# Kernel tuning notes

Measured on AMD Instinct MI355X. Metric: run time of the kernel, lower is better.

The kernel has to match this reference:

```python
import jax, jax.numpy as jnp
import numpy as np

LOG2 = float(np.log(2.0))
INV_SQRT3 = float(1.0 / np.sqrt(3.0))

def ssp(x):
    # ShiftedSoftPlus: softplus(x) - log(2)
    return jax.nn.softplus(x) - LOG2

def setup_inputs() -> dict:
    key = jax.random.key(0)
    ks = jax.random.split(key, 13)
    N, E, M, A, R, H = 50000, 800000, 32, 16, 8, 64
    return {
        "node_feats": jax.random.normal(ks[0], (N, 4 * M), dtype=jnp.float32),  # 32x0e + 32x1o flat
        "node_attrs": jax.random.normal(ks[1], (N, A), dtype=jnp.float32),
        "edge_embedding": jax.random.uniform(ks[2], (E, R), dtype=jnp.float32),  # radial basis, 0e
        "edge_attrs": jax.random.normal(ks[3], (E, 4), dtype=jnp.float32),  # SH: 1x0e + 1x1o
        "edge_index": jax.random.randint(ks[4], (2, E), 0, N),
        "W1s": jax.random.normal(ks[5], (M, M), dtype=jnp.float32),
        "W1v": jax.random.normal(ks[6], (M, M), dtype=jnp.float32),
        "Wr0": jax.random.normal(ks[7], (R, H), dtype=jnp.float32),
        "Wr1": jax.random.normal(ks[8], (H, 4 * M), dtype=jnp.float32),  # tp.weight_numel = 4 paths * 32 mul
        "W2s": jax.random.normal(ks[9], (2 * M, M), dtype=jnp.float32),
        "W2v": jax.random.normal(ks[10], (2 * M, M), dtype=jnp.float32),
        "Wsc_s": jax.random.normal(ks[11], (M, A, M), dtype=jnp.float32),
        "Wsc_v": jax.random.normal(ks[12], (M, A, M), dtype=jnp.float32),
    }

def reference(node_feats, node_attrs, edge_embedding, edge_attrs, edge_index,
              W1s, W1v, Wr0, Wr1, W2s, W2v, Wsc_s, Wsc_v):
    N = node_feats.shape[0]
    M = 32           # multiplicity of each irrep
    A = node_attrs.shape[1]
    AVG_NEIGH = 16.0
    # split flat irreps features: [N,32] scalars (0e), [N,32,3] vectors (1o)
    s_in = node_feats[:, :M]
    v_in = node_feats[:, M:].reshape(N, M, 3)

    # linear_1: per-irrep channel mixing, e3nn 1/sqrt(fan_in) normalization
    inv_m = 1.0 / float(np.sqrt(M))
    s = (s_in @ W1s) * inv_m                                  # [N,32]
    v = jnp.einsum('nmc,mk->nkc', v_in, W1v) * inv_m          # [N,32,3]

    # radial MLP on edge scalars -> per-edge tensor-product path weights [E,4,32]
    h = ssp((edge_embedding @ Wr0) * (1.0 / float(np.sqrt(edge_embedding.shape[1]))))
    w = (h @ Wr1) * (1.0 / float(np.sqrt(h.shape[1])))
    w = w.reshape(-1, 4, M)
    w0, w1, w2, w3 = w[:, 0], w[:, 1], w[:, 2], w[:, 3]

    src, dst = edge_index[0], edge_index[1]
    ss = s[src]                                               # [E,32]
    vv = v[src]                                               # [E,32,3]
    e0 = edge_attrs[:, :1]                                    # [E,1]  Y_0
    e1 = edge_attrs[:, 1:4]                                   # [E,3]  Y_1

    # weighted CG tensor product, 'uvu' paths (component normalization)
    m0 = w0 * ss * e0                                                   # 0e x 0e -> 0e
    m3 = w3 * jnp.einsum('emc,ec->em', vv, e1) * INV_SQRT3              # 1o x 1o -> 0e
    m1 = w1[:, :, None] * ss[:, :, None] * e1[:, None, :]               # 0e x 1o -> 1o
    m2 = w2[:, :, None] * vv * e0[:, :, None]                           # 1o x 0e -> 1o
    mid_s = jnp.concatenate([m0, m3], axis=1)                           # [E,64]
    mid_v = jnp.concatenate([m1, m2], axis=1)                           # [E,64,3]

    # scatter-sum to destination nodes
    ns = jax.ops.segment_sum(mid_s, dst, num_segments=N)
    nv = jax.ops.segment_sum(mid_v, dst, num_segments=N)
    neigh = 1.0 / float(np.sqrt(AVG_NEIGH))

    # linear_2 on simplified mid irreps 64x0e + 64x1o
    inv2 = 1.0 / float(np.sqrt(2 * M))
    out_s = (ns @ W2s) * (inv2 * neigh)
    out_v = jnp.einsum('nmc,mk->nkc', nv, W2v) * (inv2 * neigh)

    # self connection: FullyConnectedTensorProduct(node_feats_in, node_attrs)
    fc = 1.0 / float(np.sqrt(M * A))
    out_s = out_s + jnp.einsum('nu,na,uaw->nw', s_in, node_attrs, Wsc_s) * fc
    out_v = out_v + jnp.einsum('nuc,na,uaw->nwc', v_in, node_attrs, Wsc_v) * fc

    return jnp.concatenate([out_s, out_v.reshape(N, 3 * M)], axis=1)
```

## Files before the change

### kernel.cpp

```cpp
#include <hip/hip_runtime.h>
#include <stdint.h>
#include <math.h>

typedef __attribute__((ext_vector_type(8))) short bf16x8;
typedef __attribute__((ext_vector_type(4))) short s16x4;
typedef __attribute__((ext_vector_type(4))) float f32x4;

__device__ __forceinline__ unsigned short f2bf(float f){
  unsigned int u = __float_as_uint(f);
  u += 0x7fffu + ((u >> 16) & 1u);
  return (unsigned short)(u >> 16);
}

__device__ __forceinline__ float bf2f(short s){
  return __uint_as_float(((unsigned int)(unsigned short)s) << 16);
}

__device__ __forceinline__ float ssp_f(float x){
  float u = exp2f(-fabsf(x)*1.4426950408889634f);
  return fmaxf(x, 0.f) + 0.6931471805599453f*(__log2f(1.0f + u) - 1.0f);
}

__global__ void k_count_prep(const int* __restrict__ eidx, int E, int* __restrict__ cnt,
                             const float* __restrict__ Wr0, const float* __restrict__ Wr1,
                             const float* __restrict__ Wsc_s, const float* __restrict__ Wsc_v,
                             const float* __restrict__ W1s, const float* __restrict__ W1v,
                             const float* __restrict__ W2s, const float* __restrict__ W2v,
                             unsigned short* __restrict__ wr1frag, float* __restrict__ wr0p,
                             unsigned short* __restrict__ wscfrag, unsigned short* __restrict__ w1frag,
                             unsigned short* __restrict__ w2frag){
  int id = blockIdx.x*256 + threadIdx.x;
  if(id < 512) wr0p[id] = Wr0[(id & 7)*64 + (id >> 3)];
  if(id < 1024){
    int fi = id >> 6, lane = id & 63;
    int c0 = lane & 15, g = lane >> 4;
    int kt = fi >> 3, ct = fi & 7;
    unsigned short tmp[8];
    #pragma unroll
    for(int i = 0; i < 8; i++){
      int k = kt*32 + g*8 + i;
      tmp[i] = f2bf(Wr1[k*128 + ct*16 + c0]);
    }
    #pragma unroll
    for(int i = 0; i < 8; i++) wr1frag[id*8 + i] = tmp[i];
  }
  if(id < 4096){
    int sel  = id >> 11;
    int fi   = (id >> 6) & 31;
    int lane = id & 63;
    int c0 = lane & 15, g = lane >> 4;
    int ks = fi >> 1, ct = fi & 1;
    const float* W = sel ? Wsc_v : Wsc_s;
    bf16x8 tmp;
    #pragma unroll
    for(int i = 0; i < 8; i++){
      int k = ks*32 + g*8 + i;
      tmp[i] = (short)f2bf(W[k*32 + ct*16 + c0]);
    }
    *(bf16x8*)&wscfrag[(size_t)id*8] = tmp;
  }
  if(id < 256){
    int sel = id >> 7, ct = (id >> 6) & 1, lane = id & 63;
    int c0 = lane & 15, g = lane >> 4;
    const float* W = sel ? W1v : W1s;
    bf16x8 tmp;
    #pragma unroll
    for(int i = 0; i < 8; i++){
      int m = g*8 + i;
      tmp[i] = (short)f2bf(W[m*32 + ct*16 + c0]);
    }
    *(bf16x8*)&w1frag[(size_t)id*8] = tmp;
  }
  if(id < 512){
    int fi = id >> 6, lane = id & 63;
    int c0 = lane & 15, g = lane >> 4;
    int sel = fi >> 2, kt = (fi >> 1) & 1, ct = fi & 1;
    const float* W = sel ? W2v : W2s;
    bf16x8 tmp;
    #pragma unroll
    for(int i = 0; i < 8; i++){
      int k = kt*32 + g*8 + i;
      tmp[i] = (short)f2bf(W[k*32 + ct*16 + c0]);
    }
    *(bf16x8*)&w2frag[(size_t)id*8] = tmp;
  }
  if(id < E) atomicAdd(&cnt[eidx[E + id]], 1);
}

__global__ void k_scan_a(const int* __restrict__ cnt, int N, int* __restrict__ offs, int* __restrict__ bsum){
  __shared__ int arr[1024];
  int t = threadIdx.x, i = blockIdx.x*1024 + t;
  int v = (i < N) ? cnt[i] : 0;
  int own = v;
  arr[t] = v;
  for(int off = 1; off < 1024; off <<= 1){
    __syncthreads();
    int u = (t >= off) ? arr[t - off] : 0;
    __syncthreads();
    arr[t] += u;
  }
  if(i < N) offs[i] = arr[t] - own;
  if(t == 1023) bsum[blockIdx.x] = arr[1023];
}

__global__ void k_scan_b(int* __restrict__ bsum, int NB, int* __restrict__ offs, int N){
  if(threadIdx.x == 0 && blockIdx.x == 0){
    int run = 0;
    for(int b = 0; b < NB; b++){ int t = bsum[b]; bsum[b] = run; run += t; }
    offs[N] = run;
  }
}

__global__ void k_scan_c(int* __restrict__ offs, const int* __restrict__ bsum, int* __restrict__ cursor, int N){
  int i = blockIdx.x*1024 + threadIdx.x;
  if(i < N){
    int v = offs[i] + bsum[blockIdx.x];
    offs[i] = v;
    cursor[i] = v;
  }
}

__global__ void k_perm(const float* __restrict__ eemb, const float* __restrict__ eattr,
                       const int* __restrict__ eidx, int E, int* __restrict__ cursor,
                       int* __restrict__ src_perm, float* __restrict__ eattr_perm,
                       float* __restrict__ eemb_perm){
  int e = blockIdx.x*256 + threadIdx.x;
  if(e < E){
    int d = eidx[E + e];
    int dp = atomicAdd(&cursor[d], 1);
    src_perm[dp] = eidx[e];
    *(f32x4*)(eattr_perm + (size_t)dp*4) = *(const f32x4*)(eattr + (size_t)e*4);
    *(f32x4*)(eemb_perm + (size_t)dp*8)     = *(const f32x4*)(eemb + (size_t)e*8);
    *(f32x4*)(eemb_perm + (size_t)dp*8 + 4) = *(const f32x4*)(eemb + (size_t)e*8 + 4);
  }
}

__global__ __launch_bounds__(256) void k_node(
    const float* __restrict__ nf, const float* __restrict__ na,
    const unsigned short* __restrict__ w1frag,
    const unsigned short* __restrict__ wscfrag,
    unsigned short* __restrict__ sv, float* __restrict__ out, int N)
{
  __shared__ float xl[64*133];
  __shared__ __align__(16) float al[64*20];
  const int t = threadIdx.x;
  const int n0 = blockIdx.x*64;

  for(int idx = t; idx < 64*128; idx += 256){
    int r = idx >> 7, c = idx & 127;
    int n = n0 + r;
    xl[r*133 + c] = (n < N) ? nf[(size_t)n*128 + c] : 0.f;
  }
  for(int idx = t; idx < 64*16; idx += 256){
    int r = idx >> 4, c = idx & 15;
    int n = n0 + r;
    al[r*20 + c] = (n < N) ? na[(size_t)n*16 + c] : 0.f;
  }
  __syncthreads();

  const float INVM = 0.17677669529663689f;
  const float FC   = 0.044194173824159216f;

  const int lane = t & 63, wv = t >> 6;
  const int c0 = lane & 15, g = lane >> 4;

  {
    const unsigned short* w1f = w1frag + (size_t)((wv == 0) ? 0 : 1024);
    bf16x8 b0 = *(const bf16x8*)&w1f[(0*64 + lane)*8];
    bf16x8 b1 = *(const bf16x8*)&w1f[(1*64 + lane)*8];
    #pragma unroll
    for(int rt = 0; rt < 4; rt++){
      int row = rt*16 + c0;
      bf16x8 a;
      #pragma unroll
      for(int i = 0; i < 8; i++){
        int m = g*8 + i;
        float xv = (wv == 0) ? xl[row*133 + m] : xl[row*133 + 32 + 3*m + (wv-1)];
        a[i] = (short)f2bf(xv);
      }
      f32x4 z = {0.f,0.f,0.f,0.f};
      f32x4 d0 = __builtin_amdgcn_mfma_f32_16x16x32_bf16(a, b0, z, 0, 0, 0);
      f32x4 d1 = __builtin_amdgcn_mfma_f32_16x16x32_bf16(a, b1, z, 0, 0, 0);
      #pragma unroll
      for(int r = 0; r < 4; r++){
        int node = n0 + rt*16 + g*4 + r;
        if(node < N){
          sv[(size_t)node*128 + c0*8 + wv*2 + 0] = f2bf(d0[r]*INVM);
          sv[(size_t)node*128 + c0*8 + wv*2 + 1] = f2bf(d1[r]*INVM);
        }
      }
    }
  }

  const unsigned short* wf = wscfrag + (size_t)((wv == 0) ? 0 : 16384);

  f32x4 accm[4][2];
  #pragma unroll
  for(int rt = 0; rt < 4; rt++)
    #pragma unroll
    for(int ct = 0; ct < 2; ct++) accm[rt][ct] = (f32x4){0.f,0.f,0.f,0.f};

  for(int ks = 0; ks < 16; ks++){
    bf16x8 bfr[2];
    bfr[0] = *(const bf16x8*)&wf[(size_t)((ks*2 + 0)*64 + lane)*8];
    bfr[1] = *(const bf16x8*)&wf[(size_t)((ks*2 + 1)*64 + lane)*8];
    int u2 = ks*2 + (g >> 1);
    int ab = (g & 1)*8;
    #pragma unroll
    for(int rt = 0; rt < 4; rt++){
      int row = rt*16 + c0;
      float xv = (wv == 0) ? xl[row*133 + u2] : xl[row*133 + 32 + 3*u2 + (wv-1)];
      f32x4 v0 = *(const f32x4*)&al[row*20 + ab];
      f32x4 v1 = *(const f32x4*)&al[row*20 + ab + 4];
      bf16x8 a;
      a[0] = (short)f2bf(xv*v0[0]); a[1] = (short)f2bf(xv*v0[1]);
      a[2] = (short)f2bf(xv*v0[2]); a[3] = (short)f2bf(xv*v0[3]);
      a[4] = (short)f2bf(xv*v1[0]); a[5] = (short)f2bf(xv*v1[1]);
      a[6] = (short)f2bf(xv*v1[2]); a[7] = (short)f2bf(xv*v1[3]);
      #pragma unroll
      for(int ct = 0; ct < 2; ct++)
        accm[rt][ct] = __builtin_amdgcn_mfma_f32_16x16x32_bf16(a, bfr[ct], accm[rt][ct], 0, 0, 0);
    }
  }

  #pragma unroll
  for(int rt = 0; rt < 4; rt++)
    #pragma unroll
    for(int ct = 0; ct < 2; ct++)
      #pragma unroll
      for(int i = 0; i < 4; i++){
        int node = n0 + rt*16 + g*4 + i;
        if(node < N){
          int col = ct*16 + c0;
          float v = accm[rt][ct][i] * FC;
          if(wv == 0) out[(size_t)node*128 + col] = v;
          else        out[(size_t)node*128 + 32 + 3*col + (wv-1)] = v;
        }
      }
}

__global__ __launch_bounds__(256, 4) void k_wedge(
    const float* __restrict__ eemb_perm,
    const unsigned short* __restrict__ wr1frag, const float* __restrict__ wr0p,
    unsigned short* __restrict__ wper, int NB16, int E)
{
  __shared__ __align__(16) float wr0t[512];
  __shared__ __align__(16) unsigned short bwl[8192];
  const int t = threadIdx.x;
  {
    const f32x4* s4 = (const f32x4*)wr1frag;
    f32x4* d4 = (f32x4*)bwl;
    #pragma unroll
    for(int i = 0; i < 4; i++) d4[t + i*256] = s4[t + i*256];
    if(t < 128) ((f32x4*)wr0t)[t] = ((const f32x4*)wr0p)[t];
  }
  __syncthreads();

  const int lane = t & 63;
  const int wv   = t >> 6;
  const int c0   = lane & 15;
  const int g    = lane >> 4;
  const float S8 = 0.35355339059327373f;

  int p = blockIdx.x*4 + wv;
  if(p >= NB16) return;
  int p16 = p*16;
  int bc = E - p16; if(bc > 16) bc = 16;
  bool val = (c0 < bc);

  size_t row = (size_t)(p16 + (val ? c0 : 0))*8;
  f32x4 p0 = *(const f32x4*)(eemb_perm + row);
  f32x4 p1 = *(const f32x4*)(eemb_perm + row + 4);
  float ee[8];
  ee[0]=p0[0]; ee[1]=p0[1]; ee[2]=p0[2]; ee[3]=p0[3];
  ee[4]=p1[0]; ee[5]=p1[1]; ee[6]=p1[2]; ee[7]=p1[3];

  bf16x8 afr[2];
  #pragma unroll
  for(int kt = 0; kt < 2; kt++){
    bf16x8 a;
    #pragma unroll
    for(int i = 0; i < 8; i++){
      int j = kt*32 + g*8 + i;
      f32x4 wa = *(const f32x4*)&wr0t[j*8];
      f32x4 wb = *(const f32x4*)&wr0t[j*8 + 4];
      float pre = ee[0]*wa[0] + ee[1]*wa[1] + ee[2]*wa[2] + ee[3]*wa[3]
                + ee[4]*wb[0] + ee[5]*wb[1] + ee[6]*wb[2] + ee[7]*wb[3];
      a[i] = (short)f2bf(ssp_f(pre * S8));
    }
    afr[kt] = a;
  }

  f32x4 cfr[8];
  #pragma unroll
  for(int ct = 0; ct < 8; ct++) cfr[ct] = (f32x4){0.f,0.f,0.f,0.f};
  #pragma unroll
  for(int kt = 0; kt < 2; kt++)
    #pragma unroll
    for(int ct = 0; ct < 8; ct++){
      bf16x8 bfr = *(const bf16x8*)&bwl[((kt*8 + ct)*64 + lane)*8];
      cfr[ct] = __builtin_amdgcn_mfma_f32_16x16x32_bf16(afr[kt], bfr, cfr[ct], 0, 0, 0);
    }

  #pragma unroll
  for(int i = 0; i < 4; i++){
    if(g*4 + i < bc){
      bf16x8 wpk;
      #pragma unroll
      for(int ct = 0; ct < 8; ct++) wpk[ct] = (short)f2bf(cfr[ct][i] * 0.125f);
      *(bf16x8*)(wper + (size_t)(p16 + g*4 + i)*128 + c0*8) = wpk;
    }
  }
}

__global__ __launch_bounds__(256, 4) void k_msg(
    const unsigned short* __restrict__ sv, const unsigned short* __restrict__ wper,
    const float* __restrict__ eattr_perm, const int* __restrict__ src_perm,
    const int* __restrict__ offs, unsigned short* __restrict__ nsv, int N)
{
  __shared__ __align__(16) float nsl[4][256];
  const int t = threadIdx.x, lane = t & 63, wv = t >> 6;
  const int c0 = lane & 15, g = lane >> 4;

  const int n = blockIdx.x*4 + wv;
  if(n >= N) return;

  const float IS3 = 0.57735026918962576f;

  float acc[16];
  #pragma unroll
  for(int i = 0; i < 16; i++) acc[i] = 0.f;

  const int eb0 = offs[n], eb1 = offs[n+1];
  for(int eb = eb0; eb < eb1; eb += 16){
    int bc = eb1 - eb; if(bc > 16) bc = 16;
    #pragma unroll
    for(int r = 0; r < 4; r++){
      int es = r*4 + g;
      if(es >= bc) continue;
      int e = eb + es;
      int s = src_perm[e];
      bf16x8 sr = *(const bf16x8*)(sv + (size_t)s*128 + c0*8);
      f32x4 ea = *(const f32x4*)(eattr_perm + (size_t)e*4);
      bf16x8 w8 = *(const bf16x8*)(wper + (size_t)e*128 + c0*8);
      float w0A = bf2f(w8[0]), w0B = bf2f(w8[1]);
      float w1A = bf2f(w8[2]), w1B = bf2f(w8[3]);
      float w2A = bf2f(w8[4]), w2B = bf2f(w8[5]);
      float w3A = bf2f(w8[6]), w3B = bf2f(w8[7]);
      float ssA = bf2f(sr[0]), ssB = bf2f(sr[1]);
      float vA0 = bf2f(sr[2]), vB0 = bf2f(sr[3]);
      float vA1 = bf2f(sr[4]), vB1 = bf2f(sr[5]);
      float vA2 = bf2f(sr[6]), vB2 = bf2f(sr[7]);
      float e0 = ea[0], e1x = ea[1], e1y = ea[2], e1z = ea[3];

      acc[0] += w0A*ssA*e0;
      acc[1] += w0B*ssB*e0;
      acc[2] += w3A*(vA0*e1x + vA1*e1y + vA2*e1z);
      acc[3] += w3B*(vB0*e1x + vB1*e1y + vB2*e1z);
      float h1A = w1A*ssA, h1B = w1B*ssB;
      acc[4]  += h1A*e1x; acc[5]  += h1A*e1y; acc[6]  += h1A*e1z;
      acc[7]  += h1B*e1x; acc[8]  += h1B*e1y; acc[9]  += h1B*e1z;
      float h2A = w2A*e0, h2B = w2B*e0;
      acc[10] += h2A*vA0; acc[11] += h2A*vA1; acc[12] += h2A*vA2;
      acc[13] += h2B*vB0; acc[14] += h2B*vB1; acc[15] += h2B*vB2;
    }
  }

  #pragma unroll
  for(int i = 0; i < 16; i++){
    acc[i] += __shfl_xor(acc[i], 16);
    acc[i] += __shfl_xor(acc[i], 32);
  }

  float* nl = nsl[wv];
  if(g == 0){
    nl[c0]      = acc[0];
    nl[16 + c0] = acc[1];
    nl[32 + c0] = acc[2]*IS3;
    nl[48 + c0] = acc[3]*IS3;
    #pragma unroll
    for(int cc = 0; cc < 3; cc++){
      nl[64 + cc*64 +  0 + c0] = acc[4  + cc];
      nl[64 + cc*64 + 16 + c0] = acc[7  + cc];
      nl[64 + cc*64 + 32 + c0] = acc[10 + cc];
      nl[64 + cc*64 + 48 + c0] = acc[13 + cc];
    }
  }
  __threadfence_block();

  f32x4 v4 = *(const f32x4*)&nl[lane*4];
  s16x4 o4;
  o4[0] = (short)f2bf(v4[0]); o4[1] = (short)f2bf(v4[1]);
  o4[2] = (short)f2bf(v4[2]); o4[3] = (short)f2bf(v4[3]);
  *(s16x4*)(nsv + (size_t)n*256 + lane*4) = o4;
}

__global__ __launch_bounds__(256) void k_out(
    const unsigned short* __restrict__ nsv, const unsigned short* __restrict__ w2frag,
    float* __restrict__ out, int N)
{
  const int t = threadIdx.x, lane = t & 63, wv = t >> 6;
  const int c0 = lane & 15, g = lane >> 4;
  const int n0 = blockIdx.x*64;
  const float SC2 = 0.03125f;
  const int sel = (wv == 0) ? 0 : 1;

  bf16x8 bfr[2][2];
  #pragma unroll
  for(int kt = 0; kt < 2; kt++)
    #pragma unroll
    for(int ct = 0; ct < 2; ct++)
      bfr[kt][ct] = *(const bf16x8*)&w2frag[(size_t)(((sel*2 + kt)*2 + ct)*64 + lane)*8];

  #pragma unroll
  for(int rt = 0; rt < 4; rt++){
    int na_ = n0 + rt*16 + c0; if(na_ >= N) na_ = N - 1;
    const unsigned short* ap = nsv + (size_t)na_*256 + wv*64;
    bf16x8 a0 = *(const bf16x8*)(ap + g*8);
    bf16x8 a1 = *(const bf16x8*)(ap + 32 + g*8);
    f32x4 accq[2];
    #pragma unroll
    for(int ct = 0; ct < 2; ct++){
      f32x4 z = {0.f,0.f,0.f,0.f};
      f32x4 d = __builtin_amdgcn_mfma_f32_16x16x32_bf16(a0, bfr[0][ct], z, 0, 0, 0);
      d = __builtin_amdgcn_mfma_f32_16x16x32_bf16(a1, bfr[1][ct], d, 0, 0, 0);
      accq[ct] = d;
    }
    #pragma unroll
    for(int ct = 0; ct < 2; ct++)
      #pragma unroll
      for(int i = 0; i < 4; i++){
        int node = n0 + rt*16 + g*4 + i;
        if(node < N){
          int col = ct*16 + c0;
          size_t idx = (size_t)node*128 + ((wv == 0) ? col : 32 + 3*col + (wv-1));
          out[idx] += accq[ct][i]*SC2;
        }
      }
  }
}

extern "C" void kernel_launch(void* const* d_in, const int* in_sizes, int n_in,
                              void* d_out, int out_size, void* d_ws, size_t ws_size,
                              hipStream_t stream)
{
  const float* nf    = (const float*)d_in[0];
  const float* na    = (const float*)d_in[1];
  const float* eemb  = (const float*)d_in[2];
  const float* eattr = (const float*)d_in[3];
  const int*   eidx  = (const int*)d_in[4];
  const float* W1s   = (const float*)d_in[5];
  const float* W1v   = (const float*)d_in[6];
  const float* Wr0   = (const float*)d_in[7];
  const float* Wr1   = (const float*)d_in[8];
  const float* W2s   = (const float*)d_in[9];
  const float* W2v   = (const float*)d_in[10];
  const float* Wsc_s = (const float*)d_in[11];
  const float* Wsc_v = (const float*)d_in[12];
  float* out = (float*)d_out;

  int N = in_sizes[0]/128;
  int E = in_sizes[2]/8;
  int NB16 = (E + 15)/16;

  char* ws = (char*)d_ws;
  size_t off = 0;
  unsigned short* sv = (unsigned short*)(ws + off); off += (size_t)N*128*2;
  unsigned short* wper = (unsigned short*)(ws + off); off += (size_t)NB16*16*128*2;
  float* eemb_perm = (float*)(ws + off);      off += (size_t)NB16*16*8*4;
  unsigned short* nsv = (unsigned short*)eemb_perm;
  float* eattr_perm = (float*)(ws + off);     off += (size_t)NB16*16*4*4;
  int* src_perm = (int*)(ws + off);           off += (size_t)NB16*16*4;
  int* cnt    = (int*)(ws + off);             off += (size_t)N*4;
  int* offs   = (int*)(ws + off);             off += (size_t)(N+1)*4;
  int* cursor = (int*)(ws + off);             off += (size_t)N*4;
  int* bsum   = (int*)(ws + off);             off += 4096;
  unsigned short* wr1frag = (unsigned short*)(ws + off); off += 16384;
  float* wr0p = (float*)(ws + off);           off += 2048;
  unsigned short* wscfrag = (unsigned short*)(ws + off); off += 65536;
  unsigned short* w1frag = (unsigned short*)(ws + off);  off += 4096;
  unsigned short* w2frag = (unsigned short*)(ws + off);  off += 8192;

  int NB = (N + 1023)/1024;

  (void)hipMemsetAsync(cnt, 0, (size_t)N*4, stream);
  k_count_prep<<<dim3((E+255)/256), dim3(256), 0, stream>>>(eidx, E, cnt, Wr0, Wr1,
                                                            Wsc_s, Wsc_v, W1s, W1v, W2s, W2v,
                                                            wr1frag, wr0p, wscfrag, w1frag, w2frag);
  k_scan_a <<<dim3(NB),          dim3(1024),0, stream>>>(cnt, N, offs, bsum);
  k_scan_b <<<dim3(1),           dim3(64),  0, stream>>>(bsum, NB, offs, N);
  k_scan_c <<<dim3(NB),          dim3(1024),0, stream>>>(offs, bsum, cursor, N);
  k_perm   <<<dim3((E+255)/256), dim3(256), 0, stream>>>(eemb, eattr, eidx, E, cursor,
                                                         src_perm, eattr_perm, eemb_perm);
  k_node   <<<dim3((N+63)/64),   dim3(256), 0, stream>>>(nf, na, w1frag, wscfrag, sv, out, N);
  k_wedge  <<<dim3((NB16+3)/4),  dim3(256), 0, stream>>>(eemb_perm, wr1frag, wr0p, wper, NB16, E);
  k_msg    <<<dim3((N+3)/4),     dim3(256), 0, stream>>>(sv, wper, eattr_perm, src_perm, offs,
                                                         nsv, N);
  k_out    <<<dim3((N+63)/64),   dim3(256), 0, stream>>>(nsv, w2frag, out, N);
}
```

Before: 343.3 us.

## Fuse second radial-MLP matmul into message kernel and pack edge data in bf16

```diff
diff --git a/kernel.cpp b/kernel.cpp
--- a/kernel.cpp
+++ b/kernel.cpp
@@ -5,6 +5,7 @@
 typedef __attribute__((ext_vector_type(8))) short bf16x8;
 typedef __attribute__((ext_vector_type(4))) short s16x4;
 typedef __attribute__((ext_vector_type(4))) float f32x4;
+typedef __attribute__((ext_vector_type(4))) unsigned int u32x4;
 
 __device__ __forceinline__ unsigned short f2bf(float f){
   unsigned int u = __float_as_uint(f);
@@ -122,16 +123,24 @@
 
 __global__ void k_perm(const float* __restrict__ eemb, const float* __restrict__ eattr,
                        const int* __restrict__ eidx, int E, int* __restrict__ cursor,
-                       int* __restrict__ src_perm, float* __restrict__ eattr_perm,
-                       float* __restrict__ eemb_perm){
+                       unsigned short* __restrict__ edata){
   int e = blockIdx.x*256 + threadIdx.x;
   if(e < E){
     int d = eidx[E + e];
     int dp = atomicAdd(&cursor[d], 1);
-    src_perm[dp] = eidx[e];
-    *(f32x4*)(eattr_perm + (size_t)dp*4) = *(const f32x4*)(eattr + (size_t)e*4);
-    *(f32x4*)(eemb_perm + (size_t)dp*8)     = *(const f32x4*)(eemb + (size_t)e*8);
-    *(f32x4*)(eemb_perm + (size_t)dp*8 + 4) = *(const f32x4*)(eemb + (size_t)e*8 + 4);
+    f32x4 a = *(const f32x4*)(eemb + (size_t)e*8);
+    f32x4 b = *(const f32x4*)(eemb + (size_t)e*8 + 4);
+    bf16x8 pk;
+    pk[0] = (short)f2bf(a[0]); pk[1] = (short)f2bf(a[1]);
+    pk[2] = (short)f2bf(a[2]); pk[3] = (short)f2bf(a[3]);
+    pk[4] = (short)f2bf(b[0]); pk[5] = (short)f2bf(b[1]);
+    pk[6] = (short)f2bf(b[2]); pk[7] = (short)f2bf(b[3]);
+    f32x4 ea = *(const f32x4*)(eattr + (size_t)e*4);
+    unsigned int i0 = (unsigned int)f2bf(ea[0]) | ((unsigned int)f2bf(ea[1]) << 16);
+    unsigned int i1 = (unsigned int)f2bf(ea[2]) | ((unsigned int)f2bf(ea[3]) << 16);
+    u32x4 hi = { i0, i1, (unsigned int)eidx[e], 0u };
+    *(bf16x8*)(edata + (size_t)dp*16) = pk;
+    *(u32x4*)(edata + (size_t)dp*16 + 8) = hi;
   }
 }
 
@@ -240,20 +249,13 @@
 }
 
 __global__ __launch_bounds__(256, 4) void k_wedge(
-    const float* __restrict__ eemb_perm,
-    const unsigned short* __restrict__ wr1frag, const float* __restrict__ wr0p,
-    unsigned short* __restrict__ wper, int NB16, int E)
+    const unsigned short* __restrict__ edata,
+    const float* __restrict__ wr0p,
+    unsigned short* __restrict__ hper, int NB16, int E)
 {
   __shared__ __align__(16) float wr0t[512];
-  __shared__ __align__(16) unsigned short bwl[8192];
   const int t = threadIdx.x;
-  {
-    const f32x4* s4 = (const f32x4*)wr1frag;
-    f32x4* d4 = (f32x4*)bwl;
-    #pragma unroll
-    for(int i = 0; i < 4; i++) d4[t + i*256] = s4[t + i*256];
-    if(t < 128) ((f32x4*)wr0t)[t] = ((const f32x4*)wr0p)[t];
-  }
+  if(t < 128) ((f32x4*)wr0t)[t] = ((const f32x4*)wr0p)[t];
   __syncthreads();
 
   const int lane = t & 63;
@@ -268,14 +270,11 @@
   int bc = E - p16; if(bc > 16) bc = 16;
   bool val = (c0 < bc);
 
-  size_t row = (size_t)(p16 + (val ? c0 : 0))*8;
-  f32x4 p0 = *(const f32x4*)(eemb_perm + row);
-  f32x4 p1 = *(const f32x4*)(eemb_perm + row + 4);
+  bf16x8 eb8 = *(const bf16x8*)(edata + (size_t)(p16 + (val ? c0 : 0))*16);
   float ee[8];
-  ee[0]=p0[0]; ee[1]=p0[1]; ee[2]=p0[2]; ee[3]=p0[3];
-  ee[4]=p1[0]; ee[5]=p1[1]; ee[6]=p1[2]; ee[7]=p1[3];
-
-  bf16x8 afr[2];
+  #pragma unroll
+  for(int i = 0; i < 8; i++) ee[i] = bf2f(eb8[i]);
+
   #pragma unroll
   for(int kt = 0; kt < 2; kt++){
     bf16x8 a;
@@ -288,61 +287,101 @@
                 + ee[4]*wb[0] + ee[5]*wb[1] + ee[6]*wb[2] + ee[7]*wb[3];
       a[i] = (short)f2bf(ssp_f(pre * S8));
     }
-    afr[kt] = a;
-  }
-
-  f32x4 cfr[8];
-  #pragma unroll
-  for(int ct = 0; ct < 8; ct++) cfr[ct] = (f32x4){0.f,0.f,0.f,0.f};
-  #pragma unroll
-  for(int kt = 0; kt < 2; kt++)
+    if(val)
+      *(bf16x8*)(hper + (size_t)(p16 + c0)*64 + kt*32 + g*8) = a;
+  }
+}
+
+__global__ __launch_bounds__(256, 4) void k_msg(
+    const unsigned short* __restrict__ sv, const unsigned short* __restrict__ hper,
+    const unsigned short* __restrict__ edata, const int* __restrict__ offs,
+    const unsigned short* __restrict__ wr1frag,
+    unsigned short* __restrict__ nsv, int N)
+{
+  __shared__ __align__(16) float nsl[4][256];
+  __shared__ __align__(16) unsigned short bwl[8192];
+  __shared__ __align__(16) unsigned short wtile[4][2048];
+  const int t = threadIdx.x, lane = t & 63, wv = t >> 6;
+  const int c0 = lane & 15, g = lane >> 4;
+
+  {
+    const f32x4* s4 = (const f32x4*)wr1frag;
+    f32x4* d4 = (f32x4*)bwl;
+    #pragma unroll
+    for(int i = 0; i < 4; i++) d4[t + i*256] = s4[t + i*256];
+  }
+  __syncthreads();
+
+  const int n = blockIdx.x*4 + wv;
+  if(n >= N) return;
+
+  const float IS3 = 0.57735026918962576f;
+
+  float acc[16];
+  #pragma unroll
+  for(int i = 0; i < 16; i++) acc[i] = 0.f;
+
+  unsigned short* wt = &wtile[wv][0];
+
+  const int eb0 = offs[n], eb1 = offs[n+1];
+  for(int eb = eb0; eb < eb1; eb += 16){
+    int bc = eb1 - eb; if(bc > 16) bc = 16;
+
+    int e0i = eb + (( 0 + g) < bc ? ( 0 + g) : 0);
+    int e1i = eb + (( 4 + g) < bc ? ( 4 + g) : 0);
+    int e2i = eb + (( 8 + g) < bc ? ( 8 + g) : 0);
+    int e3i = eb + ((12 + g) < bc ? (12 + g) : 0);
+    u32x4 rec0 = *(const u32x4*)(edata + (size_t)e0i*16 + 8);
+    u32x4 rec1 = *(const u32x4*)(edata + (size_t)e1i*16 + 8);
+    u32x4 rec2 = *(const u32x4*)(edata + (size_t)e2i*16 + 8);
+    u32x4 rec3 = *(const u32x4*)(edata + (size_t)e3i*16 + 8);
+
+    int ec = eb + (c0 < bc ? c0 : 0);
+    bf16x8 a0h = *(const bf16x8*)(hper + (size_t)ec*64 + g*8);
+    bf16x8 a1h = *(const bf16x8*)(hper + (size_t)ec*64 + 32 + g*8);
+
+    bf16x8 sr0 = *(const bf16x8*)(sv + (size_t)(int)rec0.z*128 + c0*8);
+    bf16x8 sr1 = *(const bf16x8*)(sv + (size_t)(int)rec1.z*128 + c0*8);
+    bf16x8 sr2 = *(const bf16x8*)(sv + (size_t)(int)rec2.z*128 + c0*8);
+    bf16x8 sr3 = *(const bf16x8*)(sv + (size_t)(int)rec3.z*128 + c0*8);
+
+    f32x4 cfr[8];
+    #pragma unroll
+    for(int ct = 0; ct < 8; ct++) cfr[ct] = (f32x4){0.f,0.f,0.f,0.f};
     #pragma unroll
     for(int ct = 0; ct < 8; ct++){
-      bf16x8 bfr = *(const bf16x8*)&bwl[((kt*8 + ct)*64 + lane)*8];
-      cfr[ct] = __builtin_amdgcn_mfma_f32_16x16x32_bf16(afr[kt], bfr, cfr[ct], 0, 0, 0);
-    }
-
-  #pragma unroll
-  for(int i = 0; i < 4; i++){
-    if(g*4 + i < bc){
+      bf16x8 b0 = *(const bf16x8*)&bwl[((0*8 + ct)*64 + lane)*8];
+      cfr[ct] = __builtin_amdgcn_mfma_f32_16x16x32_bf16(a0h, b0, cfr[ct], 0, 0, 0);
+    }
+    #pragma unroll
+    for(int ct = 0; ct < 8; ct++){
+      bf16x8 b1 = *(const bf16x8*)&bwl[((1*8 + ct)*64 + lane)*8];
+      cfr[ct] = __builtin_amdgcn_mfma_f32_16x16x32_bf16(a1h, b1, cfr[ct], 0, 0, 0);
+    }
+
+    #pragma unroll
+    for(int i = 0; i < 4; i++){
       bf16x8 wpk;
       #pragma unroll
       for(int ct = 0; ct < 8; ct++) wpk[ct] = (short)f2bf(cfr[ct][i] * 0.125f);
-      *(bf16x8*)(wper + (size_t)(p16 + g*4 + i)*128 + c0*8) = wpk;
-    }
-  }
-}
-
-__global__ __launch_bounds__(256, 4) void k_msg(
-    const unsigned short* __restrict__ sv, const unsigned short* __restrict__ wper,
-    const float* __restrict__ eattr_perm, const int* __restrict__ src_perm,
-    const int* __restrict__ offs, unsigned short* __restrict__ nsv, int N)
-{
-  __shared__ __align__(16) float nsl[4][256];
-  const int t = threadIdx.x, lane = t & 63, wv = t >> 6;
-  const int c0 = lane & 15, g = lane >> 4;
-
-  const int n = blockIdx.x*4 + wv;
-  if(n >= N) return;
-
-  const float IS3 = 0.57735026918962576f;
-
-  float acc[16];
-  #pragma unroll
-  for(int i = 0; i < 16; i++) acc[i] = 0.f;
-
-  const int eb0 = offs[n], eb1 = offs[n+1];
-  for(int eb = eb0; eb < eb1; eb += 16){
-    int bc = eb1 - eb; if(bc > 16) bc = 16;
+      *(bf16x8*)&wt[(g*4 + i)*128 + c0*8] = wpk;
+    }
+    bf16x8 w80 = *(const bf16x8*)&wt[(0*4 + g)*128 + c0*8];
+    bf16x8 w81 = *(const bf16x8*)&wt[(1*4 + g)*128 + c0*8];
+    bf16x8 w82 = *(const bf16x8*)&wt[(2*4 + g)*128 + c0*8];
+    bf16x8 w83 = *(const bf16x8*)&wt[(3*4 + g)*128 + c0*8];
+
     #pragma unroll
     for(int r = 0; r < 4; r++){
       int es = r*4 + g;
       if(es >= bc) continue;
-      int e = eb + es;
-      int s = src_perm[e];
-      bf16x8 sr = *(const bf16x8*)(sv + (size_t)s*128 + c0*8);
-      f32x4 ea = *(const f32x4*)(eattr_perm + (size_t)e*4);
-      bf16x8 w8 = *(const bf16x8*)(wper + (size_t)e*128 + c0*8);
+      u32x4  rec = (r == 0) ? rec0 : (r == 1) ? rec1 : (r == 2) ? rec2 : rec3;
+      bf16x8 w8  = (r == 0) ? w80  : (r == 1) ? w81  : (r == 2) ? w82  : w83;
+      bf16x8 sr  = (r == 0) ? sr0  : (r == 1) ? sr1  : (r == 2) ? sr2  : sr3;
+      float e0  = bf2f((short)(rec.x & 0xffff));
+      float e1x = bf2f((short)(rec.x >> 16));
+      float e1y = bf2f((short)(rec.y & 0xffff));
+      float e1z = bf2f((short)(rec.y >> 16));
       float w0A = bf2f(w8[0]), w0B = bf2f(w8[1]);
       float w1A = bf2f(w8[2]), w1B = bf2f(w8[3]);
       float w2A = bf2f(w8[4]), w2B = bf2f(w8[5]);
@@ -351,7 +390,6 @@
       float vA0 = bf2f(sr[2]), vB0 = bf2f(sr[3]);
       float vA1 = bf2f(sr[4]), vB1 = bf2f(sr[5]);
       float vA2 = bf2f(sr[6]), vB2 = bf2f(sr[7]);
-      float e0 = ea[0], e1x = ea[1], e1y = ea[2], e1z = ea[3];
 
       acc[0] += w0A*ssA*e0;
       acc[1] += w0B*ssB*e0;
@@ -466,11 +504,9 @@
   char* ws = (char*)d_ws;
   size_t off = 0;
   unsigned short* sv = (unsigned short*)(ws + off); off += (size_t)N*128*2;
-  unsigned short* wper = (unsigned short*)(ws + off); off += (size_t)NB16*16*128*2;
-  float* eemb_perm = (float*)(ws + off);      off += (size_t)NB16*16*8*4;
-  unsigned short* nsv = (unsigned short*)eemb_perm;
-  float* eattr_perm = (float*)(ws + off);     off += (size_t)NB16*16*4*4;
-  int* src_perm = (int*)(ws + off);           off += (size_t)NB16*16*4;
+  unsigned short* edata = (unsigned short*)(ws + off); off += (size_t)NB16*16*32;
+  unsigned short* hper = (unsigned short*)(ws + off); off += (size_t)NB16*16*64*2;
+  unsigned short* nsv = (unsigned short*)(ws + off);  off += (size_t)N*256*2;
   int* cnt    = (int*)(ws + off);             off += (size_t)N*4;
   int* offs   = (int*)(ws + off);             off += (size_t)(N+1)*4;
   int* cursor = (int*)(ws + off);             off += (size_t)N*4;
@@ -490,11 +526,9 @@
   k_scan_a <<<dim3(NB),          dim3(1024),0, stream>>>(cnt, N, offs, bsum);
   k_scan_b <<<dim3(1),           dim3(64),  0, stream>>>(bsum, NB, offs, N);
   k_scan_c <<<dim3(NB),          dim3(1024),0, stream>>>(offs, bsum, cursor, N);
-  k_perm   <<<dim3((E+255)/256), dim3(256), 0, stream>>>(eemb, eattr, eidx, E, cursor,
-                                                         src_perm, eattr_perm, eemb_perm);
+  k_perm   <<<dim3((E+255)/256), dim3(256), 0, stream>>>(eemb, eattr, eidx, E, cursor, edata);
   k_node   <<<dim3((N+63)/64),   dim3(256), 0, stream>>>(nf, na, w1frag, wscfrag, sv, out, N);
-  k_wedge  <<<dim3((NB16+3)/4),  dim3(256), 0, stream>>>(eemb_perm, wr1frag, wr0p, wper, NB16, E);
-  k_msg    <<<dim3((N+3)/4),     dim3(256), 0, stream>>>(sv, wper, eattr_perm, src_perm, offs,
-                                                         nsv, N);
+  k_wedge  <<<dim3((NB16+3)/4),  dim3(256), 0, stream>>>(edata, wr0p, hper, NB16, E);
+  k_msg    <<<dim3((N+3)/4),     dim3(256), 0, stream>>>(sv, hper, edata, offs, wr1frag, nsv, N);
   k_out    <<<dim3((N+63)/64),   dim3(256), 0, stream>>>(nsv, w2frag, out, N);
 }
```

Measured after the change: 429.8 us. 1.25x slower.
